# Kernel tuning notes

Measured on AMD Instinct MI355X. Metric: run time of the kernel, lower is better.

## Reference

```python
import jax, jax.numpy as jnp
import numpy as np

N_NODES = 100000
N_EDGES = 1600000
D_FEAT = 64
D_OUT = 64


def setup_inputs() -> dict:
    key = jax.random.key(0)
    k1, k2, k3, k4 = jax.random.split(key, 4)
    vertices = jax.random.normal(k1, (N_NODES, D_FEAT), dtype=jnp.float32)
    edges = jax.random.randint(k2, (2, N_EDGES), 0, N_NODES, dtype=jnp.int64)
    weight = jax.random.normal(k3, (D_OUT, D_FEAT), dtype=jnp.float32) * (1.0 / np.sqrt(D_FEAT))
    bias = jax.random.normal(k4, (D_OUT,), dtype=jnp.float32) * 0.01
    return {"vertices": vertices, "edges": edges, "weight": weight, "bias": bias}


def reference(vertices, edges, weight, bias):
    # GraphConv forward, dense (non-sparse) path, self_loop=True, normalize=True.
    n_vertices = vertices.shape[0]
    idx = jnp.arange(n_vertices, dtype=edges.dtype)
    dst = jnp.concatenate([edges[0], idx])  # scatter destinations (edges[0])
    src = jnp.concatenate([edges[1], idx])  # gather sources (edges[1])
    # agg[i] = sum over edges with dst==i of vertices[src]
    agg = jax.ops.segment_sum(vertices[src], dst, num_segments=n_vertices)
    # degree per node (torch scatters ones_like(neighbours): all feature cols equal)
    deg = jax.ops.segment_sum(
        jnp.ones_like(dst, dtype=vertices.dtype), dst, num_segments=n_vertices
    )
    agg = agg * (jnp.clip(deg, 1.0, None) ** -0.5)[:, None]
    # Linear: y = agg @ W.T + b
    return agg @ weight.T + bias
```

## Files before the change

### kernel.cpp

```cpp
#include <hip/hip_runtime.h>
#include <hip/hip_fp16.h>

constexpr int N_NODES = 100000;
constexpr int N_EDGES = 1600000;
constexpr int D = 64;

constexpr int SHC    = 9;
constexpr int BSZC   = 1 << SHC;
constexpr int NBC    = (N_NODES + BSZC - 1) / BSZC;
constexpr int SPLITB = 256;
constexpr int TILE   = (N_EDGES + SPLITB - 1) / SPLITB;
constexpr int LINB   = 2048;
constexpr int TILE2  = 8192;
constexpr int NBLK2  = (N_EDGES + TILE2 - 1) / TILE2;

constexpr int SCAN_CHUNK = 1024;
constexpr int NCHUNK = (N_NODES + SCAN_CHUNK - 1) / SCAN_CHUNK;

__device__ __forceinline__ int waveInclScan(int v, int lane) {
    #pragma unroll
    for (int off = 1; off < 64; off <<= 1) {
        int t = __shfl_up(v, off, 64);
        if (lane >= off) v += t;
    }
    return v;
}

__global__ __launch_bounds__(256) void lin_hist(
    const float* __restrict__ vertices,
    const float* __restrict__ weight,
    __half* __restrict__ Yh,
    const int* __restrict__ edges,
    int* __restrict__ bcntC)
{
    if (blockIdx.x < LINB) {
        __shared__ float rowbuf[4][64];
        const int wid  = threadIdx.x >> 6;
        const int lane = threadIdx.x & 63;

        float w[64];
        #pragma unroll
        for (int f = 0; f < 64; ++f) w[f] = weight[lane * 64 + f];

        const int nodesPerIter = LINB * 4;
        for (int base = blockIdx.x * 4; base < N_NODES; base += nodesPerIter) {
            const int node = base + wid;
            float a = 0.0f;
            if (node < N_NODES) a = vertices[(size_t)node * D + lane];
            rowbuf[wid][lane] = a;
            __syncthreads();
            float acc = 0.0f;
            #pragma unroll
            for (int f = 0; f < 64; ++f)
                acc += rowbuf[wid][f] * w[f];
            if (node < N_NODES) Yh[(size_t)node * D + lane] = __float2half(acc);
            __syncthreads();
        }
    } else {
        __shared__ int h[NBC];
        const int b = blockIdx.x - LINB;
        if (threadIdx.x < NBC) h[threadIdx.x] = 0;
        __syncthreads();
        const int lo = b * TILE;
        const int hi = min(lo + TILE, N_EDGES);
        for (int e = lo + threadIdx.x; e < hi; e += 256)
            atomicAdd(&h[edges[e] >> SHC], 1);
        __syncthreads();
        if (threadIdx.x < NBC) {
            int v = h[threadIdx.x];
            if (v) atomicAdd(&bcntC[threadIdx.x], v);
        }
    }
}

__global__ __launch_bounds__(1024) void s_scatter(const int* __restrict__ edges,
                                                  const int* __restrict__ bcntC,
                                                  int* __restrict__ cursorDelta,
                                                  int* __restrict__ bbaseC,
                                                  int* __restrict__ packed)
{
    __shared__ int s[256];
    __shared__ int baseC[NBC];
    __shared__ int h[NBC];
    __shared__ int chunk[NBC];
    const int t = threadIdx.x;

    int v = 0;
    if (t < 256) { v = (t < NBC) ? bcntC[t] : 0; s[t] = v; }
    __syncthreads();
    for (int o = 1; o < 256; o <<= 1) {
        int u = (t < 256 && t >= o) ? s[t - o] : 0;
        __syncthreads();
        if (t < 256) s[t] += u;
        __syncthreads();
    }
    if (t < NBC) {
        int e = s[t] - v;
        baseC[t] = e;
        h[t] = 0;
        if (blockIdx.x == 0) bbaseC[t] = e;
    }
    __syncthreads();

    const int lo = blockIdx.x * TILE2;
    int myd[8];
    #pragma unroll
    for (int k = 0; k < 8; ++k) {
        int e = lo + k * 1024 + t;
        myd[k] = (e < N_EDGES) ? edges[e] : -1;
        if (myd[k] >= 0) atomicAdd(&h[myd[k] >> SHC], 1);
    }
    __syncthreads();

    if (t < NBC) {
        int c = h[t];
        chunk[t] = c ? (baseC[t] + atomicAdd(&cursorDelta[t], c)) : 0;
        h[t] = 0;
    }
    __syncthreads();

    #pragma unroll
    for (int k = 0; k < 8; ++k) {
        if (myd[k] >= 0) {
            int e = lo + k * 1024 + t;
            int src = edges[N_EDGES + e];
            int j = myd[k] >> SHC;
            int r = atomicAdd(&h[j], 1);
            packed[chunk[j] + r] = (src << SHC) | (myd[k] & (BSZC - 1));
        }
    }
}

__global__ __launch_bounds__(1024) void csr512(const int* __restrict__ packed,
                                               const int* __restrict__ bbaseC,
                                               const int* __restrict__ bcntC,
                                               int* __restrict__ offsets,
                                               int* __restrict__ deg,
                                               int* __restrict__ srt)
{
    __shared__ int h2[BSZC];
    __shared__ int cur2[BSZC];
    __shared__ int s[BSZC];
    const int b = blockIdx.x;
    const int t = threadIdx.x;
    const int start = bbaseC[b];
    const int cnt   = bcntC[b];

    if (t < BSZC) h2[t] = 0;
    __syncthreads();
    for (int i = t; i < cnt; i += 1024)
        atomicAdd(&h2[packed[start + i] & (BSZC - 1)], 1);
    __syncthreads();

    if (t < BSZC) s[t] = h2[t];
    __syncthreads();
    for (int o = 1; o < BSZC; o <<= 1) {
        int u = (t < BSZC && t >= o) ? s[t - o] : 0;
        __syncthreads();
        if (t < BSZC) s[t] += u;
        __syncthreads();
    }
    if (t < BSZC) {
        int excl = s[t] - h2[t];
        int node = (b << SHC) + t;
        if (node < N_NODES) { offsets[node] = start + excl; deg[node] = h2[t]; }
        cur2[t] = excl;
    }
    __syncthreads();
    for (int i = t; i < cnt; i += 1024) {
        int p = packed[start + i];
        int r = atomicAdd(&cur2[p & (BSZC - 1)], 1);
        srt[start + r] = p >> SHC;
    }
}

__device__ __forceinline__ void addrow(float* acc, uint4 u)
{
    const __half2* h = reinterpret_cast<const __half2*>(&u);
    #pragma unroll
    for (int k = 0; k < 4; ++k) {
        float2 f = __half22float2(h[k]);
        acc[2 * k]     += f.x;
        acc[2 * k + 1] += f.y;
    }
}

__global__ __launch_bounds__(256) void gather_h(
    const __half* __restrict__ Yh,
    const int* __restrict__ offsets,
    const int* __restrict__ deg,
    const int* __restrict__ srt,
    const float* __restrict__ bias,
    float* __restrict__ out)
{
    const int wid  = threadIdx.x >> 6;
    const int lane = threadIdx.x & 63;
    const int g    = lane >> 3;
    const int sub  = lane & 7;
    const int node = blockIdx.x * 4 + wid;
    if (node >= N_NODES) return;

    const int start = offsets[node];
    const int cnt   = deg[node];

    float acc[8];
    #pragma unroll
    for (int j = 0; j < 8; ++j) acc[j] = 0.0f;

    if (g == 0) {
        uint4 u = *reinterpret_cast<const uint4*>(Yh + (size_t)node * D + sub * 8);
        addrow(acc, u);
    }

    int e = 0;
    for (; e + 16 <= cnt; e += 16) {
        int s0 = srt[start + e + g];
        int s1 = srt[start + e + 8 + g];
        uint4 u0 = *reinterpret_cast<const uint4*>(Yh + (size_t)s0 * D + sub * 8);
        uint4 u1 = *reinterpret_cast<const uint4*>(Yh + (size_t)s1 * D + sub * 8);
        addrow(acc, u0);
        addrow(acc, u1);
    }
    if (e + 8 <= cnt) {
        int s0 = srt[start + e + g];
        uint4 u0 = *reinterpret_cast<const uint4*>(Yh + (size_t)s0 * D + sub * 8);
        addrow(acc, u0);
        e += 8;
    }
    if (e + g < cnt) {
        int s0 = srt[start + e + g];
        uint4 u0 = *reinterpret_cast<const uint4*>(Yh + (size_t)s0 * D + sub * 8);
        addrow(acc, u0);
    }

    #pragma unroll
    for (int j = 0; j < 8; ++j) {
        acc[j] += __shfl_xor(acc[j], 8, 64);
        acc[j] += __shfl_xor(acc[j], 16, 64);
        acc[j] += __shfl_xor(acc[j], 32, 64);
    }

    if (g == 0) {
        const float sc = rsqrtf((float)cnt + 1.0f);
        const float4 b0 = *reinterpret_cast<const float4*>(bias + sub * 8);
        const float4 b1 = *reinterpret_cast<const float4*>(bias + sub * 8 + 4);
        float4 r0, r1;
        r0.x = acc[0] * sc + b0.x;  r0.y = acc[1] * sc + b0.y;
        r0.z = acc[2] * sc + b0.z;  r0.w = acc[3] * sc + b0.w;
        r1.x = acc[4] * sc + b1.x;  r1.y = acc[5] * sc + b1.y;
        r1.z = acc[6] * sc + b1.z;  r1.w = acc[7] * sc + b1.w;
        *reinterpret_cast<float4*>(out + (size_t)node * D + sub * 8)     = r0;
        *reinterpret_cast<float4*>(out + (size_t)node * D + sub * 8 + 4) = r1;
    }
}


__global__ __launch_bounds__(256) void linear_kernel(
    const float* __restrict__ vertices,
    const float* __restrict__ weight,
    float* __restrict__ Y)
{
    __shared__ float rowbuf[4][64];
    const int wid  = threadIdx.x >> 6;
    const int lane = threadIdx.x & 63;
    float w[64];
    #pragma unroll
    for (int f = 0; f < 64; ++f) w[f] = weight[lane * 64 + f];
    const int nodesPerIter = gridDim.x * 4;
    for (int base = blockIdx.x * 4; base < N_NODES; base += nodesPerIter) {
        const int node = base + wid;
        float a = 0.0f;
        if (node < N_NODES) a = vertices[(size_t)node * D + lane];
        rowbuf[wid][lane] = a;
        __syncthreads();
        float acc = 0.0f;
        #pragma unroll
        for (int f = 0; f < 64; ++f)
            acc += rowbuf[wid][f] * w[f];
        if (node < N_NODES) Y[(size_t)node * D + lane] = acc;
        __syncthreads();
    }
}

__global__ __launch_bounds__(256) void gather_f32(
    const float* __restrict__ Y,
    const int* __restrict__ offsets,
    const int* __restrict__ deg,
    const int* __restrict__ sortedSrc,
    const float* __restrict__ bias,
    float* __restrict__ out)
{
    const int wid  = threadIdx.x >> 6;
    const int lane = threadIdx.x & 63;
    const int g    = lane >> 4;
    const int sub  = lane & 15;
    const int node = blockIdx.x * 4 + wid;
    if (node >= N_NODES) return;

    const int start = offsets[node];
    const int cnt   = deg[node];

    float4 acc;
    if (g == 0) {
        acc = *reinterpret_cast<const float4*>(Y + (size_t)node * D + (sub << 2));
    } else {
        acc.x = 0.0f; acc.y = 0.0f; acc.z = 0.0f; acc.w = 0.0f;
    }

    int e = 0;
    for (; e + 8 <= cnt; e += 8) {
        int s0 = sortedSrc[start + e + g];
        int s1 = sortedSrc[start + e + 4 + g];
        const float4 a0 = *reinterpret_cast<const float4*>(Y + (size_t)s0 * D + (sub << 2));
        const float4 a1 = *reinterpret_cast<const float4*>(Y + (size_t)s1 * D + (sub << 2));
        acc.x += a0.x; acc.y += a0.y; acc.z += a0.z; acc.w += a0.w;
        acc.x += a1.x; acc.y += a1.y; acc.z += a1.z; acc.w += a1.w;
    }
    if (e + 4 <= cnt) {
        int s0 = sortedSrc[start + e + g];
        const float4 a0 = *reinterpret_cast<const float4*>(Y + (size_t)s0 * D + (sub << 2));
        acc.x += a0.x; acc.y += a0.y; acc.z += a0.z; acc.w += a0.w;
        e += 4;
    }
    if (e + g < cnt) {
        int s0 = sortedSrc[start + e + g];
        const float4 a0 = *reinterpret_cast<const float4*>(Y + (size_t)s0 * D + (sub << 2));
        acc.x += a0.x; acc.y += a0.y; acc.z += a0.z; acc.w += a0.w;
    }

    acc.x += __shfl_xor(acc.x, 16, 64);
    acc.y += __shfl_xor(acc.y, 16, 64);
    acc.z += __shfl_xor(acc.z, 16, 64);
    acc.w += __shfl_xor(acc.w, 16, 64);
    acc.x += __shfl_xor(acc.x, 32, 64);
    acc.y += __shfl_xor(acc.y, 32, 64);
    acc.z += __shfl_xor(acc.z, 32, 64);
    acc.w += __shfl_xor(acc.w, 32, 64);

    if (lane < 16) {
        const float sc = rsqrtf((float)cnt + 1.0f);
        const float4 b4 = *reinterpret_cast<const float4*>(bias + (sub << 2));
        float4 r;
        r.x = acc.x * sc + b4.x;
        r.y = acc.y * sc + b4.y;
        r.z = acc.z * sc + b4.z;
        r.w = acc.w * sc + b4.w;
        *reinterpret_cast<float4*>(out + (size_t)node * D + (sub << 2)) = r;
    }
}

__global__ __launch_bounds__(256) void hist_kernel(const int* __restrict__ edges,
                                                   int* __restrict__ deg)
{
    int e = blockIdx.x * 256 + threadIdx.x;
    if (e < N_EDGES) atomicAdd(&deg[edges[e]], 1);
}

__global__ __launch_bounds__(256) void scan_part(const int* __restrict__ deg,
                                                 int* __restrict__ partial)
{
    int t = threadIdx.x;
    int base = blockIdx.x * SCAN_CHUNK + t * 4;
    int s = 0;
    #pragma unroll
    for (int k = 0; k < 4; ++k) { int i = base + k; if (i < N_NODES) s += deg[i]; }
    int lane = t & 63, wid = t >> 6;
    #pragma unroll
    for (int off = 32; off; off >>= 1) s += __shfl_down(s, off, 64);
    __shared__ int red[4];
    if (lane == 0) red[wid] = s;
    __syncthreads();
    if (t == 0) partial[blockIdx.x] = red[0] + red[1] + red[2] + red[3];
}

__global__ void scan_small(int* partial) {
    int lane = threadIdx.x;
    int v0 = (lane < NCHUNK) ? partial[lane] : 0;
    int v1 = (64 + lane < NCHUNK) ? partial[64 + lane] : 0;
    int i0 = waveInclScan(v0, lane);
    int tot0 = __shfl(i0, 63, 64);
    int i1 = waveInclScan(v1, lane) + tot0;
    if (lane < NCHUNK) partial[lane] = i0 - v0;
    if (64 + lane < NCHUNK) partial[64 + lane] = i1 - v1;
}

__global__ __launch_bounds__(256) void scan_final(const int* __restrict__ deg,
                                                  const int* __restrict__ partial,
                                                  int* __restrict__ offsets,
                                                  int* __restrict__ cursor)
{
    int t = threadIdx.x;
    int base = blockIdx.x * SCAN_CHUNK + t * 4;
    int d[4]; int s = 0;
    #pragma unroll
    for (int k = 0; k < 4; ++k) { int i = base + k; d[k] = (i < N_NODES) ? deg[i] : 0; s += d[k]; }
    __shared__ int sd[256];
    sd[t] = s; __syncthreads();
    #pragma unroll
    for (int off = 1; off < 256; off <<= 1) {
        int v = (t >= off) ? sd[t - off] : 0;
        __syncthreads();
        sd[t] += v;
        __syncthreads();
    }
    int excl = sd[t] - s + partial[blockIdx.x];
    #pragma unroll
    for (int k = 0; k < 4; ++k) {
        int i = base + k;
        if (i < N_NODES) { offsets[i] = excl; cursor[i] = excl; excl += d[k]; }
    }
}

__global__ __launch_bounds__(256) void scatter_idx(const int* __restrict__ edges,
                                                   int* __restrict__ cursor,
                                                   int* __restrict__ sortedSrc)
{
    int e = blockIdx.x * 256 + threadIdx.x;
    if (e >= N_EDGES) return;
    int dst = edges[e];
    int src = edges[N_EDGES + e];
    int pos = atomicAdd(&cursor[dst], 1);
    sortedSrc[pos] = src;
}


__global__ __launch_bounds__(256) void fb_scatter(
    const float* __restrict__ vertices, const int* __restrict__ edges,
    float* __restrict__ agg, float* __restrict__ degF)
{
    long long tid = (long long)blockIdx.x * 256 + threadIdx.x;
    int lane = threadIdx.x & 63;
    long long e = tid >> 6;
    if (e >= N_EDGES) return;
    int dst = edges[e];
    int src = edges[N_EDGES + e];
    atomicAdd(&agg[(size_t)dst * D + lane], vertices[(size_t)src * D + lane]);
    if (lane == 0) atomicAdd(&degF[dst], 1.0f);
}

__global__ __launch_bounds__(256) void fb_finish(
    const float* __restrict__ vertices, const float* __restrict__ weight,
    const float* __restrict__ bias, const float* __restrict__ degF,
    float* __restrict__ out)
{
    __shared__ float rowbuf[4][64];
    const int wid  = threadIdx.x >> 6;
    const int lane = threadIdx.x & 63;
    float w[64];
    #pragma unroll
    for (int f = 0; f < 64; ++f) w[f] = weight[lane * 64 + f];
    const float b = bias[lane];
    const int nodesPerIter = gridDim.x * 4;
    for (int base = blockIdx.x * 4; base < N_NODES; base += nodesPerIter) {
        const int node = base + wid;
        float a = 0.0f;
        if (node < N_NODES) {
            const float scale = rsqrtf(degF[node] + 1.0f);
            a = (out[(size_t)node * D + lane] + vertices[(size_t)node * D + lane]) * scale;
        }
        rowbuf[wid][lane] = a;
        __syncthreads();
        float acc = b;
        #pragma unroll
        for (int f = 0; f < 64; ++f) acc += rowbuf[wid][f] * w[f];
        if (node < N_NODES) out[(size_t)node * D + lane] = acc;
        __syncthreads();
    }
}

extern "C" void kernel_launch(void* const* d_in, const int* in_sizes, int n_in,
                              void* d_out, int out_size, void* d_ws, size_t ws_size,
                              hipStream_t stream) {
    const float* vertices = (const float*)d_in[0];
    const int*   edges    = (const int*)d_in[1];
    const float* weight   = (const float*)d_in[2];
    const float* bias     = (const float*)d_in[3];
    float* out = (float*)d_out;

    const int threads = 256;
    const int edgeBlocks = (N_EDGES + threads - 1) / threads;

    {
        __half* Yh         = (__half*)d_ws;
        int*   bcntC       = (int*)(Yh + (size_t)N_NODES * D);
        int*   cursorDelta = bcntC + NBC;
        int*   bbaseC      = cursorDelta + NBC;
        int*   offs        = bbaseC + NBC;
        int*   deg         = offs + N_NODES;
        int*   packed      = deg + N_NODES;
        int*   srt         = packed + N_EDGES;
        size_t needed      = (size_t)((char*)(srt + N_EDGES) - (char*)d_ws);
        if (ws_size >= needed) {
            hipMemsetAsync(bcntC, 0, sizeof(int) * 2 * NBC, stream);
            lin_hist<<<LINB + SPLITB, threads, 0, stream>>>(vertices, weight, Yh, edges, bcntC);
            s_scatter<<<NBLK2, 1024, 0, stream>>>(edges, bcntC, cursorDelta, bbaseC, packed);
            csr512<<<NBC, 1024, 0, stream>>>(packed, bbaseC, bcntC, offs, deg, srt);
            gather_h<<<(N_NODES + 3) / 4, threads, 0, stream>>>(Yh, offs, deg, srt, bias, out);
            return;
        }
    }

    {
        float* Y       = (float*)d_ws;
        int*   deg     = (int*)(Y + (size_t)N_NODES * D);
        int*   offs    = deg + N_NODES;
        int*   cursor  = offs + N_NODES;
        int*   partial = cursor + N_NODES;
        int*   srt     = partial + 128;
        size_t needed  = (size_t)((char*)(srt + N_EDGES) - (char*)d_ws);
        if (ws_size >= needed) {
            hipMemsetAsync(deg, 0, sizeof(int) * N_NODES, stream);
            linear_kernel<<<1024, threads, 0, stream>>>(vertices, weight, Y);
            hist_kernel<<<edgeBlocks, threads, 0, stream>>>(edges, deg);
            scan_part<<<NCHUNK, threads, 0, stream>>>(deg, partial);
            scan_small<<<1, 64, 0, stream>>>(partial);
            scan_final<<<NCHUNK, threads, 0, stream>>>(deg, partial, offs, cursor);
            scatter_idx<<<edgeBlocks, threads, 0, stream>>>(edges, cursor, srt);
            gather_f32<<<(N_NODES + 3) / 4, threads, 0, stream>>>(Y, offs, deg, srt, bias, out);
            return;
        }
    }

    {
        float* degF = (float*)d_ws;
        hipMemsetAsync(out, 0, sizeof(float) * (size_t)N_NODES * D, stream);
        hipMemsetAsync(degF, 0, sizeof(float) * N_NODES, stream);
        const long long totalScatter = (long long)N_EDGES * 64;
        fb_scatter<<<(int)((totalScatter + threads - 1) / threads), threads, 0, stream>>>(
            vertices, edges, out, degF);
        fb_finish<<<1024, threads, 0, stream>>>(vertices, weight, bias, degF, out);
    }
}
```

Before: 118.8 us.

## Halve CSR bucket size, cache packed edges in registers, use wave scans

The coarse bucket width for the two-level counting sort of edges by destination is halved, giving twice as many buckets. The per-bucket CSR kernel now runs with 512 threads, keeps up to 8 packed entries per thread in registers between the histogram and placement passes instead of re-reading global memory, and replaces the block-wide LDS Hillis-Steele scan with wave-level shuffle scans. The change also adds non-temporal loads of sorted indices and non-temporal output stores in the gather kernel, and vectorized LDS reads in the linear stage. In exchange, the histogram and scatter kernels touch more buckets, with larger shared arrays and more global atomics.

```diff
diff --git a/kernel.cpp b/kernel.cpp
--- a/kernel.cpp
+++ b/kernel.cpp
@@ -5,7 +5,9 @@
 constexpr int N_EDGES = 1600000;
 constexpr int D = 64;
 
-constexpr int SHC    = 9;
+typedef float nfloat4 __attribute__((ext_vector_type(4)));
+
+constexpr int SHC    = 8;
 constexpr int BSZC   = 1 << SHC;
 constexpr int NBC    = (N_NODES + BSZC - 1) / BSZC;
 constexpr int SPLITB = 256;
@@ -50,25 +52,28 @@
             rowbuf[wid][lane] = a;
             __syncthreads();
             float acc = 0.0f;
+            const float4* rb4 = reinterpret_cast<const float4*>(&rowbuf[wid][0]);
             #pragma unroll
-            for (int f = 0; f < 64; ++f)
-                acc += rowbuf[wid][f] * w[f];
+            for (int f4 = 0; f4 < 16; ++f4) {
+                float4 r = rb4[f4];
+                acc += r.x * w[4*f4] + r.y * w[4*f4+1] + r.z * w[4*f4+2] + r.w * w[4*f4+3];
+            }
             if (node < N_NODES) Yh[(size_t)node * D + lane] = __float2half(acc);
             __syncthreads();
         }
     } else {
         __shared__ int h[NBC];
         const int b = blockIdx.x - LINB;
-        if (threadIdx.x < NBC) h[threadIdx.x] = 0;
+        for (int i = threadIdx.x; i < NBC; i += 256) h[i] = 0;
         __syncthreads();
         const int lo = b * TILE;
         const int hi = min(lo + TILE, N_EDGES);
         for (int e = lo + threadIdx.x; e < hi; e += 256)
             atomicAdd(&h[edges[e] >> SHC], 1);
         __syncthreads();
-        if (threadIdx.x < NBC) {
-            int v = h[threadIdx.x];
-            if (v) atomicAdd(&bcntC[threadIdx.x], v);
+        for (int i = threadIdx.x; i < NBC; i += 256) {
+            int v = h[i];
+            if (v) atomicAdd(&bcntC[i], v);
         }
     }
 }
@@ -79,19 +84,19 @@
                                                   int* __restrict__ bbaseC,
                                                   int* __restrict__ packed)
 {
-    __shared__ int s[256];
+    __shared__ int s[512];
     __shared__ int baseC[NBC];
     __shared__ int h[NBC];
     __shared__ int chunk[NBC];
     const int t = threadIdx.x;
 
     int v = 0;
-    if (t < 256) { v = (t < NBC) ? bcntC[t] : 0; s[t] = v; }
-    __syncthreads();
-    for (int o = 1; o < 256; o <<= 1) {
-        int u = (t < 256 && t >= o) ? s[t - o] : 0;
-        __syncthreads();
-        if (t < 256) s[t] += u;
+    if (t < 512) { v = (t < NBC) ? bcntC[t] : 0; s[t] = v; }
+    __syncthreads();
+    for (int o = 1; o < 512; o <<= 1) {
+        int u = (t < 512 && t >= o) ? s[t - o] : 0;
+        __syncthreads();
+        if (t < 512) s[t] += u;
         __syncthreads();
     }
     if (t < NBC) {
@@ -131,16 +136,16 @@
     }
 }
 
-__global__ __launch_bounds__(1024) void csr512(const int* __restrict__ packed,
-                                               const int* __restrict__ bbaseC,
-                                               const int* __restrict__ bcntC,
-                                               int* __restrict__ offsets,
-                                               int* __restrict__ deg,
-                                               int* __restrict__ srt)
+__global__ __launch_bounds__(512) void csr256(const int* __restrict__ packed,
+                                              const int* __restrict__ bbaseC,
+                                              const int* __restrict__ bcntC,
+                                              int* __restrict__ offsets,
+                                              int* __restrict__ deg,
+                                              int* __restrict__ srt)
 {
     __shared__ int h2[BSZC];
     __shared__ int cur2[BSZC];
-    __shared__ int s[BSZC];
+    __shared__ int wtot[4];
     const int b = blockIdx.x;
     const int t = threadIdx.x;
     const int start = bbaseC[b];
@@ -148,26 +153,47 @@
 
     if (t < BSZC) h2[t] = 0;
     __syncthreads();
-    for (int i = t; i < cnt; i += 1024)
+
+    int myp[8];
+    #pragma unroll
+    for (int k = 0; k < 8; ++k) {
+        int i = k * 512 + t;
+        myp[k] = (i < cnt) ? packed[start + i] : -1;
+        if (myp[k] >= 0) atomicAdd(&h2[myp[k] & (BSZC - 1)], 1);
+    }
+    for (int i = 4096 + t; i < cnt; i += 512)
         atomicAdd(&h2[packed[start + i] & (BSZC - 1)], 1);
     __syncthreads();
 
-    if (t < BSZC) s[t] = h2[t];
-    __syncthreads();
-    for (int o = 1; o < BSZC; o <<= 1) {
-        int u = (t < BSZC && t >= o) ? s[t - o] : 0;
-        __syncthreads();
-        if (t < BSZC) s[t] += u;
-        __syncthreads();
-    }
     if (t < BSZC) {
-        int excl = s[t] - h2[t];
+        const int w    = t >> 6;
+        const int lane = t & 63;
+        int v = h2[t];
+        int incl = waveInclScan(v, lane);
+        if (lane == 63) wtot[w] = incl;
+        cur2[t] = incl - v;
+    }
+    __syncthreads();
+    if (t < BSZC) {
+        const int w = t >> 6;
+        int base = 0;
+        #pragma unroll
+        for (int ww = 0; ww < 3; ++ww) if (ww < w) base += wtot[ww];
+        int excl = cur2[t] + base;
+        cur2[t] = excl;
         int node = (b << SHC) + t;
         if (node < N_NODES) { offsets[node] = start + excl; deg[node] = h2[t]; }
-        cur2[t] = excl;
-    }
-    __syncthreads();
-    for (int i = t; i < cnt; i += 1024) {
+    }
+    __syncthreads();
+
+    #pragma unroll
+    for (int k = 0; k < 8; ++k) {
+        if (myp[k] >= 0) {
+            int r = atomicAdd(&cur2[myp[k] & (BSZC - 1)], 1);
+            srt[start + r] = myp[k] >> SHC;
+        }
+    }
+    for (int i = 4096 + t; i < cnt; i += 512) {
         int p = packed[start + i];
         int r = atomicAdd(&cur2[p & (BSZC - 1)], 1);
         srt[start + r] = p >> SHC;
@@ -214,21 +240,21 @@
 
     int e = 0;
     for (; e + 16 <= cnt; e += 16) {
-        int s0 = srt[start + e + g];
-        int s1 = srt[start + e + 8 + g];
+        int s0 = __builtin_nontemporal_load(&srt[start + e + g]);
+        int s1 = __builtin_nontemporal_load(&srt[start + e + 8 + g]);
         uint4 u0 = *reinterpret_cast<const uint4*>(Yh + (size_t)s0 * D + sub * 8);
         uint4 u1 = *reinterpret_cast<const uint4*>(Yh + (size_t)s1 * D + sub * 8);
         addrow(acc, u0);
         addrow(acc, u1);
     }
     if (e + 8 <= cnt) {
-        int s0 = srt[start + e + g];
+        int s0 = __builtin_nontemporal_load(&srt[start + e + g]);
         uint4 u0 = *reinterpret_cast<const uint4*>(Yh + (size_t)s0 * D + sub * 8);
         addrow(acc, u0);
         e += 8;
     }
     if (e + g < cnt) {
-        int s0 = srt[start + e + g];
+        int s0 = __builtin_nontemporal_load(&srt[start + e + g]);
         uint4 u0 = *reinterpret_cast<const uint4*>(Yh + (size_t)s0 * D + sub * 8);
         addrow(acc, u0);
     }
@@ -244,13 +270,13 @@
         const float sc = rsqrtf((float)cnt + 1.0f);
         const float4 b0 = *reinterpret_cast<const float4*>(bias + sub * 8);
         const float4 b1 = *reinterpret_cast<const float4*>(bias + sub * 8 + 4);
-        float4 r0, r1;
+        nfloat4 r0, r1;
         r0.x = acc[0] * sc + b0.x;  r0.y = acc[1] * sc + b0.y;
         r0.z = acc[2] * sc + b0.z;  r0.w = acc[3] * sc + b0.w;
         r1.x = acc[4] * sc + b1.x;  r1.y = acc[5] * sc + b1.y;
         r1.z = acc[6] * sc + b1.z;  r1.w = acc[7] * sc + b1.w;
-        *reinterpret_cast<float4*>(out + (size_t)node * D + sub * 8)     = r0;
-        *reinterpret_cast<float4*>(out + (size_t)node * D + sub * 8 + 4) = r1;
+        __builtin_nontemporal_store(r0, reinterpret_cast<nfloat4*>(out + (size_t)node * D + sub * 8));
+        __builtin_nontemporal_store(r1, reinterpret_cast<nfloat4*>(out + (size_t)node * D + sub * 8 + 4));
     }
 }
 
@@ -491,10 +517,10 @@
         int*   srt         = packed + N_EDGES;
         size_t needed      = (size_t)((char*)(srt + N_EDGES) - (char*)d_ws);
         if (ws_size >= needed) {
-            hipMemsetAsync(bcntC, 0, sizeof(int) * 2 * NBC, stream);
+            (void)hipMemsetAsync(bcntC, 0, sizeof(int) * 2 * NBC, stream);
             lin_hist<<<LINB + SPLITB, threads, 0, stream>>>(vertices, weight, Yh, edges, bcntC);
             s_scatter<<<NBLK2, 1024, 0, stream>>>(edges, bcntC, cursorDelta, bbaseC, packed);
-            csr512<<<NBC, 1024, 0, stream>>>(packed, bbaseC, bcntC, offs, deg, srt);
+            csr256<<<NBC, 512, 0, stream>>>(packed, bbaseC, bcntC, offs, deg, srt);
             gather_h<<<(N_NODES + 3) / 4, threads, 0, stream>>>(Yh, offs, deg, srt, bias, out);
             return;
         }
@@ -509,7 +535,7 @@
         int*   srt     = partial + 128;
         size_t needed  = (size_t)((char*)(srt + N_EDGES) - (char*)d_ws);
         if (ws_size >= needed) {
-            hipMemsetAsync(deg, 0, sizeof(int) * N_NODES, stream);
+            (void)hipMemsetAsync(deg, 0, sizeof(int) * N_NODES, stream);
             linear_kernel<<<1024, threads, 0, stream>>>(vertices, weight, Y);
             hist_kernel<<<edgeBlocks, threads, 0, stream>>>(edges, deg);
             scan_part<<<NCHUNK, threads, 0, stream>>>(deg, partial);
@@ -523,8 +549,8 @@
 
     {
         float* degF = (float*)d_ws;
-        hipMemsetAsync(out, 0, sizeof(float) * (size_t)N_NODES * D, stream);
-        hipMemsetAsync(degF, 0, sizeof(float) * N_NODES, stream);
+        (void)hipMemsetAsync(out, 0, sizeof(float) * (size_t)N_NODES * D, stream);
+        (void)hipMemsetAsync(degF, 0, sizeof(float) * N_NODES, stream);
         const long long totalScatter = (long long)N_EDGES * 64;
         fb_scatter<<<(int)((totalScatter + threads - 1) / threads), threads, 0, stream>>>(
             vertices, edges, out, degF);
```

After: 129.7 us. 9.2% more time.
